# Optimization experiments

Measured on AMD Instinct MI355X. Metric: run time of the kernel, lower is better.

## Reference

```python
import math
import jax, jax.numpy as jnp
import numpy as np

EMBED_DIM = 1024
NUM_HEADS = 16
HEAD_DIM = EMBED_DIM // NUM_HEADS  # 64


def setup_inputs() -> dict:
    key = jax.random.key(0)
    kx, kq, ko = jax.random.split(key, 3)
    B, S, D = 4, 1024, EMBED_DIM
    x = jax.random.normal(kx, (B, S, D), dtype=jnp.float32)
    # xavier_uniform for Dense kernels, zeros for biases
    def xavier(k, shape):
        fan_in, fan_out = shape[0], shape[1]
        limit = math.sqrt(6.0 / (fan_in + fan_out))
        return jax.random.uniform(k, shape, jnp.float32, -limit, limit)
    W_qkv = xavier(kq, (D, 3 * D))
    b_qkv = jnp.zeros((3 * D,), jnp.float32)
    W_o = xavier(ko, (D, D))
    b_o = jnp.zeros((D,), jnp.float32)
    return {"x": x, "W_qkv": W_qkv, "b_qkv": b_qkv, "W_o": W_o, "b_o": b_o}


def reference(x, W_qkv, b_qkv, W_o, b_o):
    B, S, D = x.shape
    H, hd = NUM_HEADS, HEAD_DIM
    qkv = x @ W_qkv + b_qkv                         # [B,S,3D]
    qkv = qkv.reshape(B, S, H, 3 * hd).transpose(0, 2, 1, 3)  # [B,H,S,3hd]
    q, k, v = jnp.split(qkv, 3, axis=-1)            # each [B,H,S,hd]
    attn_logits = jnp.einsum('bhqd,bhkd->bhqk', q, k) / math.sqrt(hd)
    attention = jax.nn.softmax(attn_logits, axis=-1)  # [B,H,S,S]
    values = jnp.einsum('bhqk,bhkd->bhqd', attention, v)
    values = values.transpose(0, 2, 1, 3).reshape(B, S, D)
    o = values @ W_o + b_o
    return (o, attention)
```

## Files before the change

kernel.cpp:

```cpp
#include <hip/hip_runtime.h>

#define B_   4
#define S_   1024
#define D_   1024
#define H_   16
#define HD_  64

typedef __bf16 bf16_t;
typedef __attribute__((ext_vector_type(8))) __bf16 bf16x8;
typedef __attribute__((ext_vector_type(4))) float f32x4;

#define MFMA16(a, b, c) __builtin_amdgcn_mfma_f32_16x16x32_bf16((a), (b), (c), 0, 0, 0)

__device__ inline unsigned short f2bf(float f) {
    unsigned int u = __builtin_bit_cast(unsigned int, f);
    u += 0x7FFFu + ((u >> 16) & 1u);
    return (unsigned short)(u >> 16);
}

__device__ inline bf16x8 ld_frag(const unsigned short* p) {
    uint4 u = *(const uint4*)p;
    return __builtin_bit_cast(bf16x8, u);
}

__global__ __launch_bounds__(256) void convert_f32_bf16(
    const float* __restrict__ in, unsigned short* __restrict__ out)
{
    const size_t idx = (size_t)blockIdx.x * 256 + threadIdx.x;
    float4 v = *(const float4*)(in + idx * 4);
    unsigned short* o = out + idx * 4;
    ushort4 r;
    r.x = f2bf(v.x); r.y = f2bf(v.y); r.z = f2bf(v.z); r.w = f2bf(v.w);
    *(ushort4*)o = r;
}

__global__ __launch_bounds__(256) void transpose_f32_bf16(
    const float* __restrict__ in, unsigned short* __restrict__ out,
    int K, int N)
{
    __shared__ float T[64][65];
    const int tid = threadIdx.x;
    const int k0 = blockIdx.y * 64, n0 = blockIdx.x * 64;
#pragma unroll
    for (int i = 0; i < 4; ++i) {
        int c = tid + i * 256;
        int row = c >> 4, col = (c & 15) << 2;
        float4 v = *(const float4*)(in + (size_t)(k0 + row) * N + n0 + col);
        T[row][col + 0] = v.x; T[row][col + 1] = v.y;
        T[row][col + 2] = v.z; T[row][col + 3] = v.w;
    }
    __syncthreads();
#pragma unroll
    for (int i = 0; i < 4; ++i) {
        int c = tid + i * 256;
        int nr = c >> 4, kc = (c & 15) << 2;
        ushort4 r;
        r.x = f2bf(T[kc + 0][nr]); r.y = f2bf(T[kc + 1][nr]);
        r.z = f2bf(T[kc + 2][nr]); r.w = f2bf(T[kc + 3][nr]);
        *(ushort4*)(out + (size_t)(n0 + nr) * K + k0 + kc) = r;
    }
}

__global__ __launch_bounds__(256) void transpose_v_bf16(
    const unsigned short* __restrict__ v,
    unsigned short* __restrict__ vt)
{
    __shared__ unsigned short T[64][65];
    const int tid = threadIdx.x;
    const int kt = blockIdx.x, bh = blockIdx.y;
    const int b = bh >> 4, h = bh & 15;
#pragma unroll
    for (int i = 0; i < 2; ++i) {
        const int c = tid + i * 256;
        const int key = c >> 3, off = (c & 7) << 3;
        uint4 u = *(const uint4*)(v + (size_t)(b * 1024 + kt * 64 + key) * 1024 + h * 64 + off);
        union { uint4 u4; unsigned short us[8]; } uu; uu.u4 = u;
#pragma unroll
        for (int t = 0; t < 8; ++t) T[key][off + t] = uu.us[t];
    }
    __syncthreads();
#pragma unroll
    for (int i = 0; i < 16; ++i) {
        const int c = tid + i * 256;
        const int dim = c >> 6, key = c & 63;
        vt[((size_t)bh * 64 + dim) * 1024 + kt * 64 + key] = T[key][dim];
    }
}

template<int MODE>
__global__ __launch_bounds__(256) void gemm_bf16(
    const unsigned short* __restrict__ A,
    const unsigned short* __restrict__ Bt,
    const float* __restrict__ bias,
    unsigned short* __restrict__ qk,
    unsigned short* __restrict__ vnat,
    float* __restrict__ out,
    int K, int N)
{
    __shared__ unsigned short Alds[128][72];
    __shared__ unsigned short Blds[128][72];
    const int tid  = threadIdx.x;
    const int l    = tid & 63, w = tid >> 6;
    const int wm   = w >> 1, wn = w & 1;
    const int quad = l >> 4, n16 = l & 15;
    const int bm = blockIdx.y * 128, bn = blockIdx.x * 128;

    const f32x4 zero4 = {0.f, 0.f, 0.f, 0.f};
    f32x4 acc[4][4];
#pragma unroll
    for (int i = 0; i < 4; ++i)
#pragma unroll
        for (int j = 0; j < 4; ++j) acc[i][j] = zero4;

    for (int k0 = 0; k0 < K; k0 += 64) {
#pragma unroll
        for (int i = 0; i < 4; ++i) {
            int c = tid + i * 256;
            int row = c >> 3, off = (c & 7) << 3;
            *(uint4*)&Alds[row][off] = *(const uint4*)(A + (size_t)(bm + row) * K + k0 + off);
            *(uint4*)&Blds[row][off] = *(const uint4*)(Bt + (size_t)(bn + row) * K + k0 + off);
        }
        __syncthreads();
#pragma unroll
        for (int kk = 0; kk < 2; ++kk) {
            const int kc = kk * 32 + quad * 8;
            bf16x8 af[4], bfv[4];
#pragma unroll
            for (int i = 0; i < 4; ++i) af[i]  = ld_frag(&Alds[wm * 64 + i * 16 + n16][kc]);
#pragma unroll
            for (int j = 0; j < 4; ++j) bfv[j] = ld_frag(&Blds[wn * 64 + j * 16 + n16][kc]);
#pragma unroll
            for (int i = 0; i < 4; ++i)
#pragma unroll
                for (int j = 0; j < 4; ++j)
                    acc[i][j] = MFMA16(af[i], bfv[j], acc[i][j]);
        }
        __syncthreads();
    }

#pragma unroll
    for (int j = 0; j < 4; ++j) {
        const int col0 = bn + wn * 64 + j * 16;
        const int col  = col0 + n16;
        const float bv = bias ? bias[col] : 0.f;
        if (MODE == 0) {
            const int head = col0 / 192;
            const int rem  = col0 % 192;
            if (rem < 128) {
                const float sc = (rem < 64) ? 0.125f : 1.0f;
#pragma unroll
                for (int i = 0; i < 4; ++i)
#pragma unroll
                    for (int r = 0; r < 4; ++r) {
                        int row = bm + wm * 64 + i * 16 + quad * 4 + r;
                        qk[(size_t)row * 2048 + head * 128 + rem + n16] =
                            f2bf((acc[i][j][r] + bv) * sc);
                    }
            } else {
                const int dcol = head * 64 + (rem - 128) + n16;
#pragma unroll
                for (int i = 0; i < 4; ++i)
#pragma unroll
                    for (int r = 0; r < 4; ++r) {
                        int row = bm + wm * 64 + i * 16 + quad * 4 + r;
                        vnat[(size_t)row * 1024 + dcol] = f2bf(acc[i][j][r] + bv);
                    }
            }
        } else {
#pragma unroll
            for (int i = 0; i < 4; ++i)
#pragma unroll
                for (int r = 0; r < 4; ++r) {
                    int row = bm + wm * 64 + i * 16 + quad * 4 + r;
                    out[(size_t)row * N + col] = acc[i][j][r] + bv;
                }
        }
    }
}

__global__ __launch_bounds__(256) void attn_fused(
    const unsigned short* __restrict__ qk,
    const unsigned short* __restrict__ vt,
    float* __restrict__ attn,
    unsigned short* __restrict__ values)
{
    __shared__ unsigned short KVw[4][2][16][72];
    __shared__ unsigned short Plds[16][1032];
    __shared__ float redbuf[2][4][16];

    const int qb = blockIdx.x, bh = blockIdx.y;
    const int b = bh >> 4, h = bh & 15;
    const int tid = threadIdx.x, l = tid & 63, w = tid >> 6;
    const int quad = l >> 4, n16 = l & 15;

    const int prow = l >> 3;
    const int poff = (l & 7) << 3;

    bf16x8 qf[2];
    {
        const unsigned short* qbase =
            qk + (size_t)(b * 1024 + qb * 16 + n16) * 2048 + h * 128 + quad * 8;
        qf[0] = ld_frag(qbase);
        qf[1] = ld_frag(qbase + 32);
    }

    const f32x4 zero4 = {0.f, 0.f, 0.f, 0.f};
    f32x4 c[16];
#pragma unroll
    for (int s = 0; s < 16; ++s) c[s] = zero4;

    const unsigned short* kwbase =
        qk + (size_t)(b * 1024 + w * 16) * 2048 + h * 128 + 64;
    {
        uint4 r0 = *(const uint4*)(kwbase + (size_t)prow * 2048 + poff);
        uint4 r1 = *(const uint4*)(kwbase + (size_t)(prow + 8) * 2048 + poff);
        *(uint4*)&KVw[w][0][prow][poff]     = r0;
        *(uint4*)&KVw[w][0][prow + 8][poff] = r1;
    }
    for (int s = 0; s < 16; ++s) {
        uint4 n0, n1;
        if (s < 15) {
            const unsigned short* p = kwbase + (size_t)(s + 1) * 64 * 2048;
            n0 = *(const uint4*)(p + (size_t)prow * 2048 + poff);
            n1 = *(const uint4*)(p + (size_t)(prow + 8) * 2048 + poff);
        }
        const int pb = s & 1;
        bf16x8 k0f = ld_frag(&KVw[w][pb][n16][quad * 8]);
        bf16x8 k1f = ld_frag(&KVw[w][pb][n16][32 + quad * 8]);
        c[s] = MFMA16(qf[0], k0f, c[s]);
        c[s] = MFMA16(qf[1], k1f, c[s]);
        if (s < 15) {
            *(uint4*)&KVw[w][pb ^ 1][prow][poff]     = n0;
            *(uint4*)&KVw[w][pb ^ 1][prow + 8][poff] = n1;
        }
    }

    float mx[4] = {-1e30f, -1e30f, -1e30f, -1e30f};
#pragma unroll
    for (int s = 0; s < 16; ++s)
#pragma unroll
        for (int r = 0; r < 4; ++r)
            mx[r] = fmaxf(mx[r], c[s][r]);
#pragma unroll
    for (int off = 1; off <= 8; off <<= 1)
#pragma unroll
        for (int r = 0; r < 4; ++r)
            mx[r] = fmaxf(mx[r], __shfl_xor(mx[r], off, 64));
    if (n16 == 0)
#pragma unroll
        for (int r = 0; r < 4; ++r) redbuf[0][w][quad * 4 + r] = mx[r];
    __syncthreads();
#pragma unroll
    for (int r = 0; r < 4; ++r) {
        const int row = quad * 4 + r;
        float m = redbuf[0][0][row];
        m = fmaxf(m, redbuf[0][1][row]);
        m = fmaxf(m, redbuf[0][2][row]);
        m = fmaxf(m, redbuf[0][3][row]);
        mx[r] = m;
    }

    float sm[4] = {0.f, 0.f, 0.f, 0.f};
#pragma unroll
    for (int s = 0; s < 16; ++s)
#pragma unroll
        for (int r = 0; r < 4; ++r) {
            float e = __expf(c[s][r] - mx[r]);
            c[s][r] = e;
            sm[r] += e;
        }
#pragma unroll
    for (int off = 1; off <= 8; off <<= 1)
#pragma unroll
        for (int r = 0; r < 4; ++r)
            sm[r] += __shfl_xor(sm[r], off, 64);
    if (n16 == 0)
#pragma unroll
        for (int r = 0; r < 4; ++r) redbuf[1][w][quad * 4 + r] = sm[r];
    __syncthreads();
    float inv[4];
#pragma unroll
    for (int r = 0; r < 4; ++r) {
        const int row = quad * 4 + r;
        inv[r] = 1.f / (redbuf[1][0][row] + redbuf[1][1][row] +
                        redbuf[1][2][row] + redbuf[1][3][row]);
    }

    float* abase = attn + ((size_t)bh * 1024 + qb * 16) * 1024;
#pragma unroll
    for (int s = 0; s < 16; ++s)
#pragma unroll
        for (int r = 0; r < 4; ++r) {
            const float a = c[s][r] * inv[r];
            const int row = quad * 4 + r;
            const int key = s * 64 + w * 16 + n16;
            abase[(size_t)row * 1024 + key] = a;
            Plds[row][key] = f2bf(a);
        }
    __syncthreads();

    f32x4 o = zero4;
    const unsigned short* vwbase = vt + (size_t)bh * 65536 +
                                   (size_t)(w * 16) * 1024;
    {
        uint4 r0 = *(const uint4*)(vwbase + (size_t)prow * 1024 + poff);
        uint4 r1 = *(const uint4*)(vwbase + (size_t)(prow + 8) * 1024 + poff);
        *(uint4*)&KVw[w][0][prow][poff]     = r0;
        *(uint4*)&KVw[w][0][prow + 8][poff] = r1;
    }
    for (int s = 0; s < 16; ++s) {
        uint4 n0, n1;
        if (s < 15) {
            const unsigned short* p = vwbase + (s + 1) * 64;
            n0 = *(const uint4*)(p + (size_t)prow * 1024 + poff);
            n1 = *(const uint4*)(p + (size_t)(prow + 8) * 1024 + poff);
        }
        const int pb = s & 1;
#pragma unroll
        for (int kk = 0; kk < 2; ++kk) {
            bf16x8 pf = ld_frag(&Plds[n16][s * 64 + kk * 32 + quad * 8]);
            bf16x8 vf = ld_frag(&KVw[w][pb][n16][kk * 32 + quad * 8]);
            o = MFMA16(pf, vf, o);
        }
        if (s < 15) {
            *(uint4*)&KVw[w][pb ^ 1][prow][poff]     = n0;
            *(uint4*)&KVw[w][pb ^ 1][prow + 8][poff] = n1;
        }
    }

#pragma unroll
    for (int r = 0; r < 4; ++r) {
        const int row = quad * 4 + r;
        values[(size_t)(b * 1024 + qb * 16 + row) * 1024 + h * 64 + w * 16 + n16] =
            f2bf(o[r]);
    }
}

extern "C" void kernel_launch(void* const* d_in, const int* in_sizes, int n_in,
                              void* d_out, int out_size, void* d_ws, size_t ws_size,
                              hipStream_t stream)
{
    const float* x     = (const float*)d_in[0];
    const float* W_qkv = (const float*)d_in[1];
    const float* b_qkv = (const float*)d_in[2];
    const float* W_o   = (const float*)d_in[3];
    const float* b_o   = (const float*)d_in[4];

    float* o_out    = (float*)d_out;
    float* attn_out = o_out + (size_t)B_ * S_ * D_;

    const size_t M1 = 1ull << 20;
    unsigned short* ws      = (unsigned short*)d_ws;
    unsigned short* x_bf    = ws;
    unsigned short* wqkvt   = ws + 4 * M1;
    unsigned short* wot     = ws + 7 * M1;
    unsigned short* qkbuf   = ws + 8 * M1;
    unsigned short* vtbuf   = ws + 16 * M1;
    unsigned short* valbuf  = ws + 20 * M1;

    convert_f32_bf16<<<4096, 256, 0, stream>>>(x, x_bf);
    transpose_f32_bf16<<<dim3(3072 / 64, 1024 / 64), 256, 0, stream>>>(W_qkv, wqkvt, 1024, 3072);
    transpose_f32_bf16<<<dim3(1024 / 64, 1024 / 64), 256, 0, stream>>>(W_o, wot, 1024, 1024);

    gemm_bf16<0><<<dim3(3072 / 128, 4096 / 128), 256, 0, stream>>>(
        x_bf, wqkvt, b_qkv, qkbuf, valbuf, nullptr, 1024, 3072);

    transpose_v_bf16<<<dim3(S_ / 64, B_ * H_), 256, 0, stream>>>(valbuf, vtbuf);

    attn_fused<<<dim3(S_ / 16, B_ * H_), 256, 0, stream>>>(
        qkbuf, vtbuf, attn_out, valbuf);

    gemm_bf16<1><<<dim3(1024 / 128, 4096 / 128), 256, 0, stream>>>(
        valbuf, wot, b_o, nullptr, nullptr, o_out, 1024, 1024);
}
```

Measured before the change: 442.2 us.

## Deepen K/V register prefetch to two stages and merge softmax max/sum reductions

The K and V tile loads in the attention kernel now prefetch two iterations ahead into registers, and the loops are fully unrolled to hide more global-memory latency. The softmax cross-wave reduction now exchanges per-wave max and sum together and rescales them online, which removes one __syncthreads and one LDS round trip. The cost is more live registers and a few extra exp operations per row, which could lower occupancy.

```diff
diff --git a/kernel.cpp b/kernel.cpp
--- a/kernel.cpp
+++ b/kernel.cpp
@@ -211,29 +211,30 @@
 
     const unsigned short* kwbase =
         qk + (size_t)(b * 1024 + w * 16) * 2048 + h * 128 + 64;
+#define KLD(S, R) (*(const uint4*)(kwbase + (size_t)((S) * 64 + (R)) * 2048 + poff))
+    uint4 pa0, pa1;
     {
-        uint4 r0 = *(const uint4*)(kwbase + (size_t)prow * 2048 + poff);
-        uint4 r1 = *(const uint4*)(kwbase + (size_t)(prow + 8) * 2048 + poff);
+        uint4 r0 = KLD(0, prow), r1 = KLD(0, prow + 8);
         *(uint4*)&KVw[w][0][prow][poff]     = r0;
         *(uint4*)&KVw[w][0][prow + 8][poff] = r1;
-    }
+        pa0 = KLD(1, prow); pa1 = KLD(1, prow + 8);
+    }
+#pragma unroll
     for (int s = 0; s < 16; ++s) {
-        uint4 n0, n1;
-        if (s < 15) {
-            const unsigned short* p = kwbase + (size_t)(s + 1) * 64 * 2048;
-            n0 = *(const uint4*)(p + (size_t)prow * 2048 + poff);
-            n1 = *(const uint4*)(p + (size_t)(prow + 8) * 2048 + poff);
-        }
+        uint4 nb0, nb1;
+        if (s < 14) { nb0 = KLD(s + 2, prow); nb1 = KLD(s + 2, prow + 8); }
         const int pb = s & 1;
         bf16x8 k0f = ld_frag(&KVw[w][pb][n16][quad * 8]);
         bf16x8 k1f = ld_frag(&KVw[w][pb][n16][32 + quad * 8]);
         c[s] = MFMA16(qf[0], k0f, c[s]);
         c[s] = MFMA16(qf[1], k1f, c[s]);
         if (s < 15) {
-            *(uint4*)&KVw[w][pb ^ 1][prow][poff]     = n0;
-            *(uint4*)&KVw[w][pb ^ 1][prow + 8][poff] = n1;
-        }
-    }
+            *(uint4*)&KVw[w][pb ^ 1][prow][poff]     = pa0;
+            *(uint4*)&KVw[w][pb ^ 1][prow + 8][poff] = pa1;
+            pa0 = nb0; pa1 = nb1;
+        }
+    }
+#undef KLD
 
     float mx[4] = {-1e30f, -1e30f, -1e30f, -1e30f};
 #pragma unroll
@@ -246,20 +247,6 @@
 #pragma unroll
         for (int r = 0; r < 4; ++r)
             mx[r] = fmaxf(mx[r], __shfl_xor(mx[r], off, 64));
-    if (n16 == 0)
-#pragma unroll
-        for (int r = 0; r < 4; ++r) redbuf[0][w][quad * 4 + r] = mx[r];
-    __syncthreads();
-#pragma unroll
-    for (int r = 0; r < 4; ++r) {
-        const int row = quad * 4 + r;
-        float m = redbuf[0][0][row];
-        m = fmaxf(m, redbuf[0][1][row]);
-        m = fmaxf(m, redbuf[0][2][row]);
-        m = fmaxf(m, redbuf[0][3][row]);
-        mx[r] = m;
-    }
-
     float sm[4] = {0.f, 0.f, 0.f, 0.f};
 #pragma unroll
     for (int s = 0; s < 16; ++s)
@@ -276,14 +263,23 @@
             sm[r] += __shfl_xor(sm[r], off, 64);
     if (n16 == 0)
 #pragma unroll
-        for (int r = 0; r < 4; ++r) redbuf[1][w][quad * 4 + r] = sm[r];
+        for (int r = 0; r < 4; ++r) {
+            redbuf[0][w][quad * 4 + r] = mx[r];
+            redbuf[1][w][quad * 4 + r] = sm[r];
+        }
     __syncthreads();
-    float inv[4];
+    float fsc[4];
 #pragma unroll
     for (int r = 0; r < 4; ++r) {
         const int row = quad * 4 + r;
-        inv[r] = 1.f / (redbuf[1][0][row] + redbuf[1][1][row] +
-                        redbuf[1][2][row] + redbuf[1][3][row]);
+        const float m0 = redbuf[0][0][row], m1 = redbuf[0][1][row];
+        const float m2 = redbuf[0][2][row], m3 = redbuf[0][3][row];
+        const float mg = fmaxf(fmaxf(m0, m1), fmaxf(m2, m3));
+        const float Z  = redbuf[1][0][row] * __expf(m0 - mg)
+                       + redbuf[1][1][row] * __expf(m1 - mg)
+                       + redbuf[1][2][row] * __expf(m2 - mg)
+                       + redbuf[1][3][row] * __expf(m3 - mg);
+        fsc[r] = __expf(mx[r] - mg) / Z;
     }
 
     float* abase = attn + ((size_t)bh * 1024 + qb * 16) * 1024;
@@ -291,7 +287,7 @@
     for (int s = 0; s < 16; ++s)
 #pragma unroll
         for (int r = 0; r < 4; ++r) {
-            const float a = c[s][r] * inv[r];
+            const float a = c[s][r] * fsc[r];
             const int row = quad * 4 + r;
             const int key = s * 64 + w * 16 + n16;
             abase[(size_t)row * 1024 + key] = a;
@@ -302,19 +298,17 @@
     f32x4 o = zero4;
     const unsigned short* vwbase = vt + (size_t)bh * 65536 +
                                    (size_t)(w * 16) * 1024;
+#define VLD(S, R) (*(const uint4*)(vwbase + (size_t)(R) * 1024 + (S) * 64 + poff))
     {
-        uint4 r0 = *(const uint4*)(vwbase + (size_t)prow * 1024 + poff);
-        uint4 r1 = *(const uint4*)(vwbase + (size_t)(prow + 8) * 1024 + poff);
+        uint4 r0 = VLD(0, prow), r1 = VLD(0, prow + 8);
         *(uint4*)&KVw[w][0][prow][poff]     = r0;
         *(uint4*)&KVw[w][0][prow + 8][poff] = r1;
-    }
+        pa0 = VLD(1, prow); pa1 = VLD(1, prow + 8);
+    }
+#pragma unroll
     for (int s = 0; s < 16; ++s) {
-        uint4 n0, n1;
-        if (s < 15) {
-            const unsigned short* p = vwbase + (s + 1) * 64;
-            n0 = *(const uint4*)(p + (size_t)prow * 1024 + poff);
-            n1 = *(const uint4*)(p + (size_t)(prow + 8) * 1024 + poff);
-        }
+        uint4 nb0, nb1;
+        if (s < 14) { nb0 = VLD(s + 2, prow); nb1 = VLD(s + 2, prow + 8); }
         const int pb = s & 1;
 #pragma unroll
         for (int kk = 0; kk < 2; ++kk) {
@@ -323,10 +317,12 @@
             o = MFMA16(pf, vf, o);
         }
         if (s < 15) {
-            *(uint4*)&KVw[w][pb ^ 1][prow][poff]     = n0;
-            *(uint4*)&KVw[w][pb ^ 1][prow + 8][poff] = n1;
-        }
-    }
+            *(uint4*)&KVw[w][pb ^ 1][prow][poff]     = pa0;
+            *(uint4*)&KVw[w][pb ^ 1][prow + 8][poff] = pa1;
+            pa0 = nb0; pa1 = nb1;
+        }
+    }
+#undef VLD
 
 #pragma unroll
     for (int r = 0; r < 4; ++r) {
```

New measurement: 452.1 us. 2.2% more time.

## Merge preprocessing kernels and register-prefetch next GEMM tile

Applied to the files above, without the earlier changes.

Folds the x conversion and the two weight transposes into one launch that dispatches on block index, removing two kernel launches. The bf16 GEMM now loads the next K-slice of A and B into registers right after the barrier, so global loads overlap the MFMA work on the current LDS tile. This costs extra VGPRs per thread, which may reduce occupancy.

```diff
diff --git a/kernel.cpp b/kernel.cpp
--- a/kernel.cpp
+++ b/kernel.cpp
@@ -23,24 +23,29 @@
     return __builtin_bit_cast(bf16x8, u);
 }
 
-__global__ __launch_bounds__(256) void convert_f32_bf16(
-    const float* __restrict__ in, unsigned short* __restrict__ out)
-{
-    const size_t idx = (size_t)blockIdx.x * 256 + threadIdx.x;
-    float4 v = *(const float4*)(in + idx * 4);
-    unsigned short* o = out + idx * 4;
-    ushort4 r;
-    r.x = f2bf(v.x); r.y = f2bf(v.y); r.z = f2bf(v.z); r.w = f2bf(v.w);
-    *(ushort4*)o = r;
-}
-
-__global__ __launch_bounds__(256) void transpose_f32_bf16(
-    const float* __restrict__ in, unsigned short* __restrict__ out,
-    int K, int N)
+__global__ __launch_bounds__(256) void preprocess(
+    const float* __restrict__ x,     unsigned short* __restrict__ x_bf,
+    const float* __restrict__ W_qkv, unsigned short* __restrict__ wqkvt,
+    const float* __restrict__ W_o,   unsigned short* __restrict__ wot)
 {
     __shared__ float T[64][65];
     const int tid = threadIdx.x;
-    const int k0 = blockIdx.y * 64, n0 = blockIdx.x * 64;
+    int bid = blockIdx.x;
+
+    if (bid < 4096) {
+        const size_t idx = (size_t)bid * 256 + tid;
+        float4 v = *(const float4*)(x + idx * 4);
+        ushort4 r;
+        r.x = f2bf(v.x); r.y = f2bf(v.y); r.z = f2bf(v.z); r.w = f2bf(v.w);
+        *(ushort4*)(x_bf + idx * 4) = r;
+        return;
+    }
+    bid -= 4096;
+    const float* in; unsigned short* out; int N, bx, by;
+    if (bid < 768) { in = W_qkv; out = wqkvt; N = 3072; bx = bid % 48; by = bid / 48; }
+    else { bid -= 768; in = W_o; out = wot; N = 1024; bx = bid % 16; by = bid / 16; }
+    const int K = 1024;
+    const int k0 = by * 64, n0 = bx * 64;
 #pragma unroll
     for (int i = 0; i < 4; ++i) {
         int c = tid + i * 256;
@@ -105,6 +110,9 @@
     const int quad = l >> 4, n16 = l & 15;
     const int bm = blockIdx.y * 128, bn = blockIdx.x * 128;
 
+    const int soff = (tid & 7) << 3;
+    const int row0 = tid >> 3;
+
     const f32x4 zero4 = {0.f, 0.f, 0.f, 0.f};
     f32x4 acc[4][4];
 #pragma unroll
@@ -112,15 +120,27 @@
 #pragma unroll
         for (int j = 0; j < 4; ++j) acc[i][j] = zero4;
 
+    uint4 pa[4], pb[4];
+#pragma unroll
+    for (int i = 0; i < 4; ++i) {
+        pa[i] = *(const uint4*)(A  + (size_t)(bm + row0 + i * 32) * K + soff);
+        pb[i] = *(const uint4*)(Bt + (size_t)(bn + row0 + i * 32) * K + soff);
+    }
+
     for (int k0 = 0; k0 < K; k0 += 64) {
 #pragma unroll
         for (int i = 0; i < 4; ++i) {
-            int c = tid + i * 256;
-            int row = c >> 3, off = (c & 7) << 3;
-            *(uint4*)&Alds[row][off] = *(const uint4*)(A + (size_t)(bm + row) * K + k0 + off);
-            *(uint4*)&Blds[row][off] = *(const uint4*)(Bt + (size_t)(bn + row) * K + k0 + off);
+            *(uint4*)&Alds[row0 + i * 32][soff] = pa[i];
+            *(uint4*)&Blds[row0 + i * 32][soff] = pb[i];
         }
         __syncthreads();
+        if (k0 + 64 < K) {
+#pragma unroll
+            for (int i = 0; i < 4; ++i) {
+                pa[i] = *(const uint4*)(A  + (size_t)(bm + row0 + i * 32) * K + k0 + 64 + soff);
+                pb[i] = *(const uint4*)(Bt + (size_t)(bn + row0 + i * 32) * K + k0 + 64 + soff);
+            }
+        }
 #pragma unroll
         for (int kk = 0; kk < 2; ++kk) {
             const int kc = kk * 32 + quad * 8;
@@ -358,9 +378,8 @@
     unsigned short* vtbuf   = ws + 16 * M1;
     unsigned short* valbuf  = ws + 20 * M1;
 
-    convert_f32_bf16<<<4096, 256, 0, stream>>>(x, x_bf);
-    transpose_f32_bf16<<<dim3(3072 / 64, 1024 / 64), 256, 0, stream>>>(W_qkv, wqkvt, 1024, 3072);
-    transpose_f32_bf16<<<dim3(1024 / 64, 1024 / 64), 256, 0, stream>>>(W_o, wot, 1024, 1024);
+    preprocess<<<4096 + 768 + 256, 256, 0, stream>>>(
+        x, x_bf, W_qkv, wqkvt, W_o, wot);
 
     gemm_bf16<0><<<dim3(3072 / 128, 4096 / 128), 256, 0, stream>>>(
         x_bf, wqkvt, b_qkv, qkbuf, valbuf, nullptr, 1024, 3072);
```

Result: slower. 548.8 us (+24.1%).
